# Kernel tuning notes

Hardware: AMD Instinct MI355X
Metric: run time of the kernel (lower is better)

## Reference

```python
import jax, jax.numpy as jnp
import numpy as np

NUM_OPS, B, T, D = 8, 8, 512, 1024


def setup_inputs() -> dict:
    key = jax.random.key(0)
    k1, k2, k3, k4 = jax.random.split(key, 4)
    x = jax.random.normal(k1, (B, T, D), dtype=jnp.float32)
    W = jax.random.normal(k2, (NUM_OPS, D, D), dtype=jnp.float32) * 0.02
    b = jnp.zeros((NUM_OPS, D), dtype=jnp.float32)
    logits = 0.001 * jax.random.normal(k3, (NUM_OPS,), dtype=jnp.float32)
    # uniform noise for Gumbel sampling (matches tf.random.uniform in sample_without_replacement)
    u = jax.random.uniform(k4, (NUM_OPS,), dtype=jnp.float32, minval=1e-6, maxval=1.0 - 1e-6)
    return {"x": x, "W": W, "b": b, "logits": logits, "u": u}


def reference(x, W, b, logits, u):
    # weights = softmax(logits); gumbel top-1 over log(weights) == log_softmax(logits)
    gumbel = -jnp.log(-jnp.log(u))
    idx = jnp.argmax(jax.nn.log_softmax(logits) + gumbel)
    # forward of ops_times_mask_binary: sum over ON ops (num_on_samples=1 -> single op)
    out = jnp.einsum('btd,de->bte', x, W[idx]) + b[idx]  # [B,T,D]
    return out
```

## Files before the change

### kernel.cpp

```cpp
#include <hip/hip_runtime.h>

typedef unsigned short u16;
typedef unsigned int u32;
typedef __attribute__((ext_vector_type(8))) short bf16x8;
typedef __attribute__((ext_vector_type(4))) float f32x4;

#define NUM_OPS 8
#define M_DIM 4096
#define K_DIM 1024
#define N_DIM 1024
#define BK 32
#define KITERS (K_DIM / BK)


__device__ __forceinline__ u16 f2b(float f) {
  union { float f; u32 u; } v; v.f = f;
  u32 r = v.u + 0x7fffu + ((v.u >> 16) & 1u);
  return (u16)(r >> 16);
}

__device__ __forceinline__ u32 pk2(float a, float b) {
  return (u32)f2b(a) | ((u32)f2b(b) << 16);
}

__device__ __forceinline__ int compute_idx(const float* __restrict__ logits,
                                           const float* __restrict__ u) {
  int best = 0; float bv = -3.4e38f;
#pragma unroll
  for (int i = 0; i < NUM_OPS; ++i) {
    float v = logits[i] - logf(-logf(u[i]));
    if (v > bv) { bv = v; best = i; }
  }
  return best;
}

__device__ __forceinline__ void gld_lds16(const void* g, void* l) {
  __builtin_amdgcn_global_load_lds(
      (__attribute__((address_space(1))) void*)(g),
      (__attribute__((address_space(3))) void*)(unsigned)(unsigned long long)(l),
      16, 0, 0);
}

__global__ void prep_kernel(const float* __restrict__ x, const float* __restrict__ W,
                            const float* __restrict__ logits, const float* __restrict__ u,
                            u16* __restrict__ xb, u16* __restrict__ wt) {
  const int tid = threadIdx.x;
  const int bid = blockIdx.x;
  if (bid < 2048) {
    const int chunk = bid * 4 + (tid >> 6), l = tid & 63;
    const int mtile = chunk >> 5, ktile = chunk & 31;
    const float* src = x + (size_t)(mtile * 16 + (l & 15)) * K_DIM
                         + ktile * 32 + (l >> 4) * 8;
    float4 f0 = *(const float4*)(src);
    float4 f1 = *(const float4*)(src + 4);
    uint4 p;
    p.x = pk2(f0.x, f0.y); p.y = pk2(f0.z, f0.w);
    p.z = pk2(f1.x, f1.y); p.w = pk2(f1.z, f1.w);
    *(uint4*)(xb + (size_t)chunk * 512 + l * 8) = p;
  } else {
    __shared__ u16 t[64][66];
    const int wb = bid - 2048;
    const int kt = wb >> 4, nt = wb & 15;
    const int idx = compute_idx(logits, u);
    const float* Wi = W + (size_t)idx * K_DIM * N_DIM;
#pragma unroll
    for (int it = 0; it < 16; ++it) {
      int i = it * 256 + tid;
      int r = i >> 6, c = i & 63;
      t[r][c] = f2b(Wi[(size_t)(kt * 64 + r) * N_DIM + nt * 64 + c]);
    }
    __syncthreads();
#pragma unroll
    for (int it = 0; it < 2; ++it) {
      int s = it * 256 + tid;
      int c = s >> 6, l = s & 63;
      int ntl = c & 3, ktl = c >> 2;
      int kb = ktl * 32 + (l >> 4) * 8, nn = ntl * 16 + (l & 15);
      uint4 p;
      p.x = (u32)t[kb + 0][nn] | ((u32)t[kb + 1][nn] << 16);
      p.y = (u32)t[kb + 2][nn] | ((u32)t[kb + 3][nn] << 16);
      p.z = (u32)t[kb + 4][nn] | ((u32)t[kb + 5][nn] << 16);
      p.w = (u32)t[kb + 6][nn] | ((u32)t[kb + 7][nn] << 16);
      int chunk = (nt * 4 + ntl) * 32 + (kt * 2 + ktl);
      *(uint4*)(wt + (size_t)chunk * 512 + l * 8) = p;
    }
  }
}

__global__ __launch_bounds__(256) void gemm_kernel(
    const u16* __restrict__ xb, const u16* __restrict__ wt,
    const float* __restrict__ bvec, const float* __restrict__ logits,
    const float* __restrict__ u, float* __restrict__ out) {
  __shared__ u16 sA[2][8 * 512];
  __shared__ u16 sB[2][8 * 512];

  const int tid = threadIdx.x;
  const int w = tid >> 6, L = tid & 63;
  const int bid = blockIdx.x;
  const int mb = (bid & 7) * 4 + (bid >> 6);
  const int nb = (bid >> 3) & 7;
  const int m0 = mb * 128, n0 = nb * 128;

  const int c0 = 2 * w, c1 = 2 * w + 1;
  const u16* gA0 = xb + ((size_t)((mb * 8 + c0) * 32)) * 512 + L * 8;
  const u16* gA1 = xb + ((size_t)((mb * 8 + c1) * 32)) * 512 + L * 8;
  const u16* gB0 = wt + ((size_t)((nb * 8 + c0) * 32)) * 512 + L * 8;
  const u16* gB1 = wt + ((size_t)((nb * 8 + c1) * 32)) * 512 + L * 8;
  const int lA0 = c0 * 512 + L * 8, lA1 = c1 * 512 + L * 8;

  const int wm = w & 1, wn = w >> 1;
  int aoff[4], boff[4];
#pragma unroll
  for (int t = 0; t < 4; ++t) {
    aoff[t] = (4 * wm + t) * 512 + L * 8;
    boff[t] = (4 * wn + t) * 512 + L * 8;
  }

  f32x4 acc[4][4] = {};

  gld_lds16(gA0, &sA[0][lA0]);
  gld_lds16(gA1, &sA[0][lA1]);
  gld_lds16(gB0, &sB[0][lA0]);
  gld_lds16(gB1, &sB[0][lA1]);

  for (int kk = 0; kk < KITERS; ++kk) {
    const int cur = kk & 1, nxt = cur ^ 1;
    __syncthreads();

    if (kk + 1 < KITERS) {
      const int ko = (kk + 1) * 512;
      gld_lds16(gA0 + ko, &sA[nxt][lA0]);
      gld_lds16(gA1 + ko, &sA[nxt][lA1]);
      gld_lds16(gB0 + ko, &sB[nxt][lA0]);
      gld_lds16(gB1 + ko, &sB[nxt][lA1]);
    }

    bf16x8 af[4], bf[4];
#pragma unroll
    for (int t = 0; t < 4; ++t) {
      af[t] = *(const bf16x8*)(&sA[cur][aoff[t]]);
      bf[t] = *(const bf16x8*)(&sB[cur][boff[t]]);
    }
#pragma unroll
    for (int mt = 0; mt < 4; ++mt)
#pragma unroll
      for (int nt = 0; nt < 4; ++nt)
        acc[mt][nt] = __builtin_amdgcn_mfma_f32_16x16x32_bf16(
            af[mt], bf[nt], acc[mt][nt], 0, 0, 0);
  }

  const int idx = compute_idx(logits, u);
  const float* bi = bvec + (size_t)idx * N_DIM;
#pragma unroll
  for (int mt = 0; mt < 4; ++mt) {
    int row = m0 + 64 * wm + 16 * mt + (L >> 4) * 4;
#pragma unroll
    for (int nt = 0; nt < 4; ++nt) {
      int col = n0 + 64 * wn + 16 * nt + (L & 15);
      float bv = bi[col];
#pragma unroll
      for (int r = 0; r < 4; ++r)
        out[(size_t)(row + r) * N_DIM + col] = acc[mt][nt][r] + bv;
    }
  }
}


extern "C" void kernel_launch(void* const* d_in, const int* in_sizes, int n_in,
                              void* d_out, int out_size, void* d_ws, size_t ws_size,
                              hipStream_t stream) {
  const float* x      = (const float*)d_in[0];
  const float* W      = (const float*)d_in[1];
  const float* bvec   = (const float*)d_in[2];
  const float* logits = (const float*)d_in[3];
  const float* u      = (const float*)d_in[4];
  float* out = (float*)d_out;

  u16* xb = (u16*)d_ws;
  u16* wt = (u16*)d_ws + (size_t)M_DIM * K_DIM;

  prep_kernel<<<2048 + 256, 256, 0, stream>>>(x, W, logits, u, xb, wt);
  gemm_kernel<<<256, 256, 0, stream>>>(xb, wt, bvec, logits, u, out);
}
```

Measured before the change: 112.2 us.

## Shrink GEMM tile to 64x128 with BK=64, doubling block count

The GEMM tile changes from 128x128 with a K step of 32 to 64x128 with a K step of 64, and the grid grows from 256 to 512 blocks. This gives the 256 CUs more than one block each and halves the number of K iterations and barriers. A and B tiles now share one LDS buffer, loaded with six async global-to-LDS copies per thread. The trade-off is less reuse per block, since each block does 8 MFMAs per K-substep instead of 16, and total global traffic for W rises.

```diff
diff --git a/kernel.cpp b/kernel.cpp
--- a/kernel.cpp
+++ b/kernel.cpp
@@ -9,7 +9,7 @@
 #define M_DIM 4096
 #define K_DIM 1024
 #define N_DIM 1024
-#define BK 32
+#define BK 64
 #define KITERS (K_DIM / BK)
 
 
@@ -91,76 +91,90 @@
     const u16* __restrict__ xb, const u16* __restrict__ wt,
     const float* __restrict__ bvec, const float* __restrict__ logits,
     const float* __restrict__ u, float* __restrict__ out) {
-  __shared__ u16 sA[2][8 * 512];
-  __shared__ u16 sB[2][8 * 512];
+  __shared__ u16 sm[2][24 * 512];
 
   const int tid = threadIdx.x;
   const int w = tid >> 6, L = tid & 63;
   const int bid = blockIdx.x;
-  const int mb = (bid & 7) * 4 + (bid >> 6);
+  const int mb = (bid & 7) * 8 + (bid >> 6);
   const int nb = (bid >> 3) & 7;
-  const int m0 = mb * 128, n0 = nb * 128;
 
-  const int c0 = 2 * w, c1 = 2 * w + 1;
-  const u16* gA0 = xb + ((size_t)((mb * 8 + c0) * 32)) * 512 + L * 8;
-  const u16* gA1 = xb + ((size_t)((mb * 8 + c1) * 32)) * 512 + L * 8;
-  const u16* gB0 = wt + ((size_t)((nb * 8 + c0) * 32)) * 512 + L * 8;
-  const u16* gB1 = wt + ((size_t)((nb * 8 + c1) * 32)) * 512 + L * 8;
-  const int lA0 = c0 * 512 + L * 8, lA1 = c1 * 512 + L * 8;
+  const u16* gsrc[6];
+  int lofs[6];
+#pragma unroll
+  for (int j = 0; j < 6; ++j) {
+    int item = 6 * w + j;
+    if (item < 8) {
+      int mt = item >> 1, dk = item & 1;
+      gsrc[j] = xb + ((size_t)((mb * 4 + mt) * 32 + dk)) * 512 + L * 8;
+    } else {
+      int t = item - 8, nt = t >> 1, dk = t & 1;
+      gsrc[j] = wt + ((size_t)((nb * 8 + nt) * 32 + dk)) * 512 + L * 8;
+    }
+    lofs[j] = item * 512 + L * 8;
+  }
 
   const int wm = w & 1, wn = w >> 1;
-  int aoff[4], boff[4];
+  int aoff[2][2], boff[4][2];
 #pragma unroll
-  for (int t = 0; t < 4; ++t) {
-    aoff[t] = (4 * wm + t) * 512 + L * 8;
-    boff[t] = (4 * wn + t) * 512 + L * 8;
-  }
+  for (int f = 0; f < 2; ++f)
+#pragma unroll
+    for (int dk = 0; dk < 2; ++dk)
+      aoff[f][dk] = ((2 * wm + f) * 2 + dk) * 512 + L * 8;
+#pragma unroll
+  for (int t = 0; t < 4; ++t)
+#pragma unroll
+    for (int dk = 0; dk < 2; ++dk)
+      boff[t][dk] = (8 + (4 * wn + t) * 2 + dk) * 512 + L * 8;
 
-  f32x4 acc[4][4] = {};
+  f32x4 acc[2][4] = {};
 
-  gld_lds16(gA0, &sA[0][lA0]);
-  gld_lds16(gA1, &sA[0][lA1]);
-  gld_lds16(gB0, &sB[0][lA0]);
-  gld_lds16(gB1, &sB[0][lA1]);
+#pragma unroll
+  for (int j = 0; j < 6; ++j) gld_lds16(gsrc[j], &sm[0][lofs[j]]);
 
   for (int kk = 0; kk < KITERS; ++kk) {
     const int cur = kk & 1, nxt = cur ^ 1;
     __syncthreads();
 
     if (kk + 1 < KITERS) {
-      const int ko = (kk + 1) * 512;
-      gld_lds16(gA0 + ko, &sA[nxt][lA0]);
-      gld_lds16(gA1 + ko, &sA[nxt][lA1]);
-      gld_lds16(gB0 + ko, &sB[nxt][lA0]);
-      gld_lds16(gB1 + ko, &sB[nxt][lA1]);
+      const int ko = (kk + 1) * 1024;
+#pragma unroll
+      for (int j = 0; j < 6; ++j) gld_lds16(gsrc[j] + ko, &sm[nxt][lofs[j]]);
     }
 
-    bf16x8 af[4], bf[4];
+    bf16x8 af[2][2], bf[4][2];
 #pragma unroll
-    for (int t = 0; t < 4; ++t) {
-      af[t] = *(const bf16x8*)(&sA[cur][aoff[t]]);
-      bf[t] = *(const bf16x8*)(&sB[cur][boff[t]]);
-    }
+    for (int f = 0; f < 2; ++f)
 #pragma unroll
-    for (int mt = 0; mt < 4; ++mt)
+      for (int dk = 0; dk < 2; ++dk)
+        af[f][dk] = *(const bf16x8*)(&sm[cur][aoff[f][dk]]);
 #pragma unroll
-      for (int nt = 0; nt < 4; ++nt)
-        acc[mt][nt] = __builtin_amdgcn_mfma_f32_16x16x32_bf16(
-            af[mt], bf[nt], acc[mt][nt], 0, 0, 0);
+    for (int t = 0; t < 4; ++t)
+#pragma unroll
+      for (int dk = 0; dk < 2; ++dk)
+        bf[t][dk] = *(const bf16x8*)(&sm[cur][boff[t][dk]]);
+#pragma unroll
+    for (int dk = 0; dk < 2; ++dk)
+#pragma unroll
+      for (int f = 0; f < 2; ++f)
+#pragma unroll
+        for (int t = 0; t < 4; ++t)
+          acc[f][t] = __builtin_amdgcn_mfma_f32_16x16x32_bf16(
+              af[f][dk], bf[t][dk], acc[f][t], 0, 0, 0);
   }
 
   const int idx = compute_idx(logits, u);
   const float* bi = bvec + (size_t)idx * N_DIM;
 #pragma unroll
-  for (int mt = 0; mt < 4; ++mt) {
-    int row = m0 + 64 * wm + 16 * mt + (L >> 4) * 4;
+  for (int f = 0; f < 2; ++f) {
+    int row = mb * 64 + 32 * wm + 16 * f + (L >> 4) * 4;
 #pragma unroll
-    for (int nt = 0; nt < 4; ++nt) {
-      int col = n0 + 64 * wn + 16 * nt + (L & 15);
+    for (int t = 0; t < 4; ++t) {
+      int col = nb * 128 + 64 * wn + 16 * t + (L & 15);
       float bv = bi[col];
 #pragma unroll
       for (int r = 0; r < 4; ++r)
-        out[(size_t)(row + r) * N_DIM + col] = acc[mt][nt][r] + bv;
+        out[(size_t)(row + r) * N_DIM + col] = acc[f][t][r] + bv;
     }
   }
 }
@@ -180,5 +194,5 @@
   u16* wt = (u16*)d_ws + (size_t)M_DIM * K_DIM;
 
   prep_kernel<<<2048 + 256, 256, 0, stream>>>(x, W, logits, u, xb, wt);
-  gemm_kernel<<<256, 256, 0, stream>>>(xb, wt, bvec, logits, u, out);
+  gemm_kernel<<<512, 256, 0, stream>>>(xb, wt, bvec, logits, u, out);
 }
```

New measurement: 105.6 us, median of 2. -5.9%, faster.

## Load A fragments directly to registers and shrink GEMM tile to 128x64

Applied to the files above, without the earlier changes.

The GEMM now loads the pre-packed A fragments straight from global memory into registers, double-buffered, instead of staging them through LDS. Only B is staged in shared memory. The block tile shrinks from 128x128 to 128x64, so 512 blocks are launched instead of 256, which raises CU occupancy and cuts LDS use. The trade-off is lower per-warp reuse (2x4 MFMA tiles instead of 4x4), more global traffic for A across N blocks, and direct register loads exposing global latency.

```diff
diff --git a/kernel.cpp b/kernel.cpp
--- a/kernel.cpp
+++ b/kernel.cpp
@@ -91,37 +91,26 @@
     const u16* __restrict__ xb, const u16* __restrict__ wt,
     const float* __restrict__ bvec, const float* __restrict__ logits,
     const float* __restrict__ u, float* __restrict__ out) {
-  __shared__ u16 sA[2][8 * 512];
-  __shared__ u16 sB[2][8 * 512];
+  __shared__ u16 sB[2][4 * 512];
 
   const int tid = threadIdx.x;
   const int w = tid >> 6, L = tid & 63;
   const int bid = blockIdx.x;
-  const int mb = (bid & 7) * 4 + (bid >> 6);
-  const int nb = (bid >> 3) & 7;
-  const int m0 = mb * 128, n0 = nb * 128;
+  const int mb = (bid & 7) * 4 + ((bid >> 3) & 3);
+  const int nb = bid >> 5;
+  const int m0 = mb * 128, n0 = nb * 64;
 
-  const int c0 = 2 * w, c1 = 2 * w + 1;
-  const u16* gA0 = xb + ((size_t)((mb * 8 + c0) * 32)) * 512 + L * 8;
-  const u16* gA1 = xb + ((size_t)((mb * 8 + c1) * 32)) * 512 + L * 8;
-  const u16* gB0 = wt + ((size_t)((nb * 8 + c0) * 32)) * 512 + L * 8;
-  const u16* gB1 = wt + ((size_t)((nb * 8 + c1) * 32)) * 512 + L * 8;
-  const int lA0 = c0 * 512 + L * 8, lA1 = c1 * 512 + L * 8;
+  const u16* gA0 = xb + ((size_t)(mb * 8 + 2 * w) * 32) * 512 + L * 8;
+  const u16* gA1 = gA0 + 32 * 512;
+  const u16* gB = wt + ((size_t)(nb * 4 + w) * 32) * 512 + L * 8;
+  const int lB = w * 512 + L * 8;
 
-  const int wm = w & 1, wn = w >> 1;
-  int aoff[4], boff[4];
-#pragma unroll
-  for (int t = 0; t < 4; ++t) {
-    aoff[t] = (4 * wm + t) * 512 + L * 8;
-    boff[t] = (4 * wn + t) * 512 + L * 8;
-  }
+  f32x4 acc[2][4] = {};
 
-  f32x4 acc[4][4] = {};
-
-  gld_lds16(gA0, &sA[0][lA0]);
-  gld_lds16(gA1, &sA[0][lA1]);
-  gld_lds16(gB0, &sB[0][lA0]);
-  gld_lds16(gB1, &sB[0][lA1]);
+  gld_lds16(gB, &sB[0][lB]);
+  bf16x8 ra[2][2];
+  ra[0][0] = *(const bf16x8*)(gA0);
+  ra[0][1] = *(const bf16x8*)(gA1);
 
   for (int kk = 0; kk < KITERS; ++kk) {
     const int cur = kk & 1, nxt = cur ^ 1;
@@ -129,38 +118,34 @@
 
     if (kk + 1 < KITERS) {
       const int ko = (kk + 1) * 512;
-      gld_lds16(gA0 + ko, &sA[nxt][lA0]);
-      gld_lds16(gA1 + ko, &sA[nxt][lA1]);
-      gld_lds16(gB0 + ko, &sB[nxt][lA0]);
-      gld_lds16(gB1 + ko, &sB[nxt][lA1]);
+      gld_lds16(gB + ko, &sB[nxt][lB]);
+      ra[nxt][0] = *(const bf16x8*)(gA0 + ko);
+      ra[nxt][1] = *(const bf16x8*)(gA1 + ko);
     }
 
-    bf16x8 af[4], bf[4];
+    bf16x8 bf[4];
 #pragma unroll
-    for (int t = 0; t < 4; ++t) {
-      af[t] = *(const bf16x8*)(&sA[cur][aoff[t]]);
-      bf[t] = *(const bf16x8*)(&sB[cur][boff[t]]);
-    }
+    for (int t = 0; t < 4; ++t) bf[t] = *(const bf16x8*)(&sB[cur][t * 512 + L * 8]);
 #pragma unroll
-    for (int mt = 0; mt < 4; ++mt)
+    for (int f = 0; f < 2; ++f)
 #pragma unroll
-      for (int nt = 0; nt < 4; ++nt)
-        acc[mt][nt] = __builtin_amdgcn_mfma_f32_16x16x32_bf16(
-            af[mt], bf[nt], acc[mt][nt], 0, 0, 0);
+      for (int t = 0; t < 4; ++t)
+        acc[f][t] = __builtin_amdgcn_mfma_f32_16x16x32_bf16(
+            ra[cur][f], bf[t], acc[f][t], 0, 0, 0);
   }
 
   const int idx = compute_idx(logits, u);
   const float* bi = bvec + (size_t)idx * N_DIM;
 #pragma unroll
-  for (int mt = 0; mt < 4; ++mt) {
-    int row = m0 + 64 * wm + 16 * mt + (L >> 4) * 4;
+  for (int f = 0; f < 2; ++f) {
+    int row = m0 + 32 * w + 16 * f + (L >> 4) * 4;
 #pragma unroll
-    for (int nt = 0; nt < 4; ++nt) {
-      int col = n0 + 64 * wn + 16 * nt + (L & 15);
+    for (int t = 0; t < 4; ++t) {
+      int col = n0 + 16 * t + (L & 15);
       float bv = bi[col];
 #pragma unroll
       for (int r = 0; r < 4; ++r)
-        out[(size_t)(row + r) * N_DIM + col] = acc[mt][nt][r] + bv;
+        out[(size_t)(row + r) * N_DIM + col] = acc[f][t][r] + bv;
     }
   }
 }
@@ -180,5 +165,5 @@
   u16* wt = (u16*)d_ws + (size_t)M_DIM * K_DIM;
 
   prep_kernel<<<2048 + 256, 256, 0, stream>>>(x, W, logits, u, xb, wt);
-  gemm_kernel<<<256, 256, 0, stream>>>(xb, wt, bvec, logits, u, out);
+  gemm_kernel<<<512, 256, 0, stream>>>(xb, wt, bvec, logits, u, out);
 }
```

Result: faster. 109.5 us (-2.5%).
